# Performance work log

Hardware: AMD Instinct MI355X
Metric: run time of the kernel (lower is better)

Reference implementation:

```python
import jax, jax.numpy as jnp
import numpy as np

N_NODES = 50000
N_EDGES = 800000
N_GRAPHS = 1024
N_PAIRS = 16384
N_CL = 16
IN_CH = 64
EMB = 128
HID = 256
OUT = 1


def _xavier(key, shape):
    fan_in, fan_out = shape[-2], shape[-1]
    lim = (6.0 / (fan_in + fan_out)) ** 0.5
    return jax.random.uniform(key, shape, jnp.float32, -lim, lim)


def setup_inputs() -> dict:
    key = jax.random.key(0)
    ks = jax.random.split(key, 12)
    x = jax.random.normal(ks[0], (N_NODES, IN_CH), jnp.float32)
    edge_index = jax.random.randint(ks[1], (2, N_EDGES), 0, N_NODES)
    batch = jnp.sort(jax.random.randint(ks[2], (N_NODES,), 0, N_GRAPHS))
    drug_drug_batch = jax.random.randint(ks[3], (2, N_PAIRS), 0, N_GRAPHS)
    edge_cell_lines = jax.random.randint(ks[4], (N_PAIRS,), 0, N_CL)
    conv1_w = _xavier(ks[5], (IN_CH, EMB))
    conv2_w = _xavier(ks[6], (EMB, EMB))
    reg_w1 = _xavier(ks[7], (N_CL, 2 * EMB, HID))
    reg_w2 = _xavier(ks[8], (N_CL, HID, OUT))
    return dict(
        x=x,
        conv1_w=conv1_w, conv1_b=jnp.zeros((EMB,), jnp.float32),
        conv2_w=conv2_w, conv2_b=jnp.zeros((EMB,), jnp.float32),
        reg_w1=reg_w1, reg_b1=jnp.zeros((N_CL, HID), jnp.float32),
        reg_w2=reg_w2, reg_b2=jnp.zeros((N_CL, OUT), jnp.float32),
        edge_index=edge_index, batch=batch,
        drug_drug_batch=drug_drug_batch, edge_cell_lines=edge_cell_lines,
    )


def _forward(x, conv1_w, conv1_b, conv2_w, conv2_b,
             reg_w1, reg_b1, reg_w2, reg_b2,
             edge_index, batch, drug_drug_batch, edge_cell_lines):
    n = x.shape[0]
    # GCN normalization with self-loops (PyG GCNConv default)
    loop = jnp.arange(n)
    row = jnp.concatenate([edge_index[0], loop])  # source
    col = jnp.concatenate([edge_index[1], loop])  # target
    deg = jax.ops.segment_sum(jnp.ones(row.shape[0], x.dtype), col, num_segments=n)
    dinv = jnp.where(deg > 0, jax.lax.rsqrt(deg), 0.0)
    norm = dinv[row] * dinv[col]  # [E+N]

    def gcn(h, W, b):
        hw = h @ W
        agg = jax.ops.segment_sum(norm[:, None] * hw[row], col, num_segments=n)
        return agg + b

    h = jax.nn.relu(gcn(x, conv1_w, conv1_b))
    h = jax.nn.relu(gcn(h, conv2_w, conv2_b))

    # scatter-mean pooling over graphs
    gsum = jax.ops.segment_sum(h, batch, num_segments=N_GRAPHS)
    cnt = jax.ops.segment_sum(jnp.ones(n, h.dtype), batch, num_segments=N_GRAPHS)
    graph_embeds = gsum / jnp.maximum(cnt, 1.0)[:, None]

    # np.digitize(ddb, unique(ddb)+1); with contiguous ids 0..G-1 this is identity,
    # expressed faithfully via searchsorted against bins = arange(G)+1
    bins = jnp.arange(N_GRAPHS) + 1
    q = jnp.searchsorted(bins, drug_drug_batch, side='right')
    pair = jnp.concatenate([graph_embeds[q[0]], graph_embeds[q[1]]], axis=1)  # [P, 2*EMB]

    # per-cell-line Linear-ReLU-Linear, computed for all lines then selected
    hcl = jax.nn.relu(jnp.einsum('pe,ceh->pch', pair, reg_w1) + reg_b1[None])  # [P,C,H]
    ocl = jnp.einsum('pch,cho->pco', hcl, reg_w2) + reg_b2[None]               # [P,C,O]
    preds = jnp.take_along_axis(ocl, edge_cell_lines[:, None, None], axis=1)[:, 0, :]
    return preds


def reference(x, conv1_w, conv1_b, conv2_w, conv2_b,
              reg_w1, reg_b1, reg_w2, reg_b2,
              edge_index, batch, drug_drug_batch, edge_cell_lines):
    return _forward(x, conv1_w, conv1_b, conv2_w, conv2_b,
                    reg_w1, reg_b1, reg_w2, reg_b2,
                    edge_index, batch, drug_drug_batch, edge_cell_lines)
```

## Files before the change

### kernel.cpp

```cpp
#include <hip/hip_runtime.h>
#include <hip/hip_fp16.h>

#define NN 50000
#define NE 800000
#define NG 1024
#define NP 16384
#define NCL 16
#define INCH 64
#define EMB 128
#define HID 256

#define NB 391
#define NCHUNK 400
#define EPB 2000

#define CDIV(a,b) (((a)+(b)-1)/(b))

typedef _Float16 f16x8 __attribute__((ext_vector_type(8)));
typedef float    f32x4 __attribute__((ext_vector_type(4)));

template<int NW>
__device__ __forceinline__ int block_excl_scan(int v, int t, int* incl_out) {
    int lane = t & 63, w = t >> 6;
    int s = v;
#pragma unroll
    for (int d = 1; d < 64; d <<= 1) {
        int u = __shfl_up(s, d, 64);
        if (lane >= d) s += u;
    }
    __shared__ int wsum[NW];
    if (lane == 63) wsum[w] = s;
    __syncthreads();
    int add = 0;
    for (int k = 0; k < w; ++k) add += wsum[k];
    *incl_out = s + add;
    return s + add - v;
}

__global__ __launch_bounds__(256) void k_cnt(const int* __restrict__ cols,
                                             int* __restrict__ cnt) {
    __shared__ int hist[NB];
    int ch = blockIdx.x, t = threadIdx.x;
    for (int b = t; b < NB; b += 256) hist[b] = 0;
    __syncthreads();
    for (int e = ch * EPB + t; e < (ch + 1) * EPB; e += 256)
        atomicAdd(&hist[cols[e] >> 7], 1);
    __syncthreads();
    for (int b = t; b < NB; b += 256) cnt[b * NCHUNK + ch] = hist[b];
}

__global__ __launch_bounds__(512) void k_bscan(int* __restrict__ cnt,
                                               int* __restrict__ btot) {
    int b = blockIdx.x, t = threadIdx.x;
    int v = (t < NCHUNK) ? cnt[b * NCHUNK + t] : 0;
    int incl;
    int excl = block_excl_scan<8>(v, t, &incl);
    if (t < NCHUNK) cnt[b * NCHUNK + t] = excl;
    if (t == NCHUNK - 1) btot[b] = incl;
}

__global__ __launch_bounds__(512) void k_btot(const int* __restrict__ btot,
                                              int* __restrict__ bbase) {
    int t = threadIdx.x;
    int v = (t < NB) ? btot[t] : 0;
    int incl;
    int excl = block_excl_scan<8>(v, t, &incl);
    if (t < NB) bbase[t] = excl;
    if (t == NB - 1) bbase[NB] = incl;
}

__global__ __launch_bounds__(256) void k_part(const int* __restrict__ rows,
                                              const int* __restrict__ cols,
                                              const int* __restrict__ cnt,
                                              const int* __restrict__ bbase,
                                              int* __restrict__ ebuf) {
    __shared__ int cur[NB];
    int ch = blockIdx.x, t = threadIdx.x;
    for (int b = t; b < NB; b += 256) cur[b] = bbase[b] + cnt[b * NCHUNK + ch];
    __syncthreads();
    for (int e = ch * EPB + t; e < (ch + 1) * EPB; e += 256) {
        int c = cols[e], r = rows[e];
        int pos = atomicAdd(&cur[c >> 7], 1);
        ebuf[pos] = (r << 7) | (c & 127);
    }
}

__global__ __launch_bounds__(256) void k_bsort(const int* __restrict__ ebuf,
                                               const int* __restrict__ bbase,
                                               const float* __restrict__ x,
                                               int* __restrict__ off,
                                               float* __restrict__ dinv,
                                               int* __restrict__ srows,
                                               __half* __restrict__ xs) {
    __shared__ int   ldeg[128];
    __shared__ int   lcur[128];
    __shared__ float ldinv[128];
    int b = blockIdx.x, t = threadIdx.x;
    int n0 = b << 7;
    int nloc = min(128, NN - n0);
    int beg = bbase[b], end = bbase[b + 1];
    if (t < 128) ldeg[t] = 0;
    __syncthreads();
    for (int i = beg + t; i < end; i += 256)
        atomicAdd(&ldeg[ebuf[i] & 127], 1);
    __syncthreads();
    int v = (t < nloc) ? ldeg[t] : 0;
    int incl;
    int excl = block_excl_scan<4>(v, t, &incl);
    if (t < nloc) {
        off[n0 + t]  = beg + excl + v;
        float d = rsqrtf((float)(v + 1));
        dinv[n0 + t] = d;
        ldinv[t] = d;
        lcur[t] = beg + excl;
    }
    __syncthreads();
    for (int i = beg + t; i < end; i += 256) {
        int e = ebuf[i];
        int pos = atomicAdd(&lcur[e & 127], 1);
        srows[pos] = e >> 7;
    }
    const float4* Xx = (const float4*)x;
#pragma unroll
    for (int i = 0; i < 8; ++i) {
        int f4 = t + i * 256;
        int rloc = f4 >> 4, kq = f4 & 15;
        if (rloc < nloc) {
            float d = ldinv[rloc];
            float4 vv = Xx[(size_t)(n0 + rloc) * 16 + kq];
            __half2 h[2];
            h[0] = __floats2half2_rn(d * vv.x, d * vv.y);
            h[1] = __floats2half2_rn(d * vv.z, d * vv.w);
            ((float2*)xs)[(size_t)(n0 + rloc) * 16 + kq] = *(float2*)h;
        }
    }
}

__global__ __launch_bounds__(256) void k_wconv(const float* __restrict__ W,
                                               __half* __restrict__ WT, int K) {
    int i = blockIdx.x * 256 + threadIdx.x;
    if (i >= K * 128) return;
    int k = i >> 7, n = i & 127;
    WT[n * K + k] = __float2half(W[i]);
}

__global__ __launch_bounds__(256) void k_wconvb(const float* __restrict__ W1,
                                                __half* __restrict__ Whl) {
    int i = blockIdx.x * 256 + threadIdx.x;
    if (i >= 32 * 256 * 16) return;
    int ch = i & 15, tg = (i >> 4) & 255, z = i >> 12;
    int c = z >> 1, part = z & 1;
    f16x8 hi, lo;
#pragma unroll
    for (int j = 0; j < 8; ++j) {
        float v = W1[(size_t)c * 65536 + (size_t)(part * 128 + ch * 8 + j) * 256 + tg];
        _Float16 h = (_Float16)v;
        hi[j] = h;
        lo[j] = (_Float16)(v - (float)h);
    }
    size_t base = ((size_t)z * 256 + tg) * 16 + ch;
    ((f16x8*)Whl)[base] = hi;
    ((f16x8*)Whl)[(size_t)32 * 256 * 16 + base] = lo;
}

template<int FEAT, bool ZB>
__global__ __launch_bounds__(256) void k_gath_h(const int* __restrict__ off,
                                                const int* __restrict__ srows,
                                                const float* __restrict__ dinv,
                                                const __half* __restrict__ SRC,
                                                __half* __restrict__ DST,
                                                float* __restrict__ zbuf) {
    if (ZB) {
        if (blockIdx.x < 512) zbuf[(blockIdx.x << 8) + threadIdx.x] = 0.f;
    }
    constexpr int NC = FEAT / 8;
    constexpr int PL = NC / 8;
    int node = blockIdx.x * 4 + (threadIdx.x >> 6);
    int lane = threadIdx.x & 63;
    int slot = lane >> 3, q = lane & 7;
    if (node >= NN) return;
    int beg = node ? off[node - 1] : 0;
    int end = off[node];
    float di = dinv[node];
    const float4* S4 = (const float4*)SRC;

    float acc[PL][8];
#pragma unroll
    for (int i = 0; i < PL; ++i)
#pragma unroll
        for (int j = 0; j < 8; ++j) acc[i][j] = 0.f;

    if (slot == 0) {
#pragma unroll
        for (int i = 0; i < PL; ++i) {
            float4 raw = S4[node * NC + i * 8 + q];
            const __half2* h = (const __half2*)&raw;
#pragma unroll
            for (int j = 0; j < 4; ++j) {
                float2 f = __half22float2(h[j]);
                acc[i][2 * j + 0] = f.x;
                acc[i][2 * j + 1] = f.y;
            }
        }
    }
    for (int e = beg + slot; e < end; e += 8) {
        int r = srows[e];
#pragma unroll
        for (int i = 0; i < PL; ++i) {
            float4 raw = S4[r * NC + i * 8 + q];
            const __half2* h = (const __half2*)&raw;
#pragma unroll
            for (int j = 0; j < 4; ++j) {
                float2 f = __half22float2(h[j]);
                acc[i][2 * j + 0] += f.x;
                acc[i][2 * j + 1] += f.y;
            }
        }
    }
#pragma unroll
    for (int d = 8; d < 64; d <<= 1)
#pragma unroll
        for (int i = 0; i < PL; ++i)
#pragma unroll
            for (int j = 0; j < 8; ++j)
                acc[i][j] += __shfl_xor(acc[i][j], d, 64);

    if (lane < 8) {
        float4* D4 = (float4*)DST;
#pragma unroll
        for (int i = 0; i < PL; ++i) {
            float4 pk;
            __half2* hp = (__half2*)&pk;
            hp[0] = __floats2half2_rn(di * acc[i][0], di * acc[i][1]);
            hp[1] = __floats2half2_rn(di * acc[i][2], di * acc[i][3]);
            hp[2] = __floats2half2_rn(di * acc[i][4], di * acc[i][5]);
            hp[3] = __floats2half2_rn(di * acc[i][6], di * acc[i][7]);
            D4[node * NC + i * 8 + lane] = pk;
        }
    }
}

template<int K, bool RS, bool POOL>
__global__ __launch_bounds__(256) void gemm_mf(const __half* __restrict__ X,
                                               const __half* __restrict__ WT,
                                               const float* __restrict__ bias,
                                               const float* __restrict__ rs,
                                               const int* __restrict__ batch,
                                               float* __restrict__ Y, int M) {
    constexpr int KP = K + 8;
    __shared__ __half Xs[64 * KP];
    __shared__ __half Ws[128 * KP];
    __shared__ int sb[64];
    const int t = threadIdx.x;
    const int row0 = blockIdx.x * 64;

    const float4* X8 = (const float4*)X;
#pragma unroll
    for (int i = t; i < 64 * (K / 8); i += 256) {
        int r = i / (K / 8), ch = i % (K / 8);
        float4 v = make_float4(0.f, 0.f, 0.f, 0.f);
        if (row0 + r < M) v = X8[(size_t)(row0 + r) * (K / 8) + ch];
        *(float4*)&Xs[r * KP + ch * 8] = v;
    }
    const float4* W8 = (const float4*)WT;
#pragma unroll
    for (int i = t; i < 128 * (K / 8); i += 256) {
        int n = i / (K / 8), ch = i % (K / 8);
        *(float4*)&Ws[n * KP + ch * 8] = W8[i];
    }
    if (POOL) {
        if (t < 64) sb[t] = (row0 + t < M) ? batch[row0 + t] : -1;
    }
    __syncthreads();

    const int w  = t >> 6;
    const int l  = t & 63;
    const int lm = l & 15, lg = l >> 4;

    f32x4 acc[8];
#pragma unroll
    for (int c = 0; c < 8; ++c) acc[c] = (f32x4){0.f, 0.f, 0.f, 0.f};

#pragma unroll
    for (int kk = 0; kk < K / 32; ++kk) {
        f16x8 a = *(const f16x8*)&Xs[(16 * w + lm) * KP + kk * 32 + lg * 8];
#pragma unroll
        for (int c = 0; c < 8; ++c) {
            f16x8 bf = *(const f16x8*)&Ws[(16 * c + lm) * KP + kk * 32 + lg * 8];
            acc[c] = __builtin_amdgcn_mfma_f32_16x16x32_f16(a, bf, acc[c], 0, 0, 0);
        }
    }

    float bcol[8];
#pragma unroll
    for (int c = 0; c < 8; ++c) bcol[c] = bias[16 * c + lm];

    if (POOL) {
#pragma unroll
        for (int c = 0; c < 8; ++c) {
            int rung = -1;
            float run = 0.f;
#pragma unroll
            for (int j = 0; j < 4; ++j) {
                int rr = 16 * w + 4 * lg + j;
                int g = (row0 + rr < M) ? sb[rr] : -1;
                if (g != rung) {
                    if (rung >= 0) atomicAdd(&Y[rung * 128 + 16 * c + lm], run);
                    run = 0.f;
                    rung = g;
                }
                if (g >= 0) run += fmaxf(acc[c][j] + bcol[c], 0.f);
            }
            if (rung >= 0) atomicAdd(&Y[rung * 128 + 16 * c + lm], run);
        }
        return;
    }

    __half* Yh = (__half*)Y;
#pragma unroll
    for (int j = 0; j < 4; ++j) {
        int r = row0 + 16 * w + 4 * lg + j;
        if (r < M) {
            float d = RS ? rs[r] : 1.f;
#pragma unroll
            for (int c = 0; c < 8; ++c) {
                float v = d * fmaxf(acc[c][j] + bcol[c], 0.f);
                Yh[(size_t)r * 128 + 16 * c + lm] = __float2half(v);
            }
        }
    }
}

__global__ __launch_bounds__(128) void k_div(const float* __restrict__ gsum,
                                             const int* __restrict__ batch,
                                             __half* __restrict__ geh) {
    int g = blockIdx.x;
    __shared__ float inv;
    if (threadIdx.x == 0) {
        int lo = 0, hi = NN;
        while (lo < hi) { int m = (lo + hi) >> 1; if (batch[m] < g) lo = m + 1; else hi = m; }
        int s = lo;
        lo = 0; hi = NN;
        while (lo < hi) { int m = (lo + hi) >> 1; if (batch[m] < g + 1) lo = m + 1; else hi = m; }
        float c = (float)(lo - s);
        inv = 1.f / fmaxf(c, 1.f);
    }
    __syncthreads();
    geh[g * 128 + threadIdx.x] = __float2half(gsum[g * 128 + threadIdx.x] * inv);
}

__global__ __launch_bounds__(256) void gemm_bat(const __half* __restrict__ GEh,
                                                const __half* __restrict__ Whl,
                                                float* __restrict__ Aarr,
                                                float* __restrict__ Barr) {
    constexpr int KP = 128 + 8;
    __shared__ __half Xs[64 * KP];
    __shared__ __half Ws[128 * KP];
    const int t = threadIdx.x;
    const int row0 = blockIdx.x * 64;
    const int y = blockIdx.y, z = blockIdx.z;

    const float4* X8 = (const float4*)GEh;
#pragma unroll
    for (int i = t; i < 64 * 16; i += 256) {
        int r = i >> 4, ch = i & 15;
        *(float4*)&Xs[r * KP + ch * 8] = X8[(size_t)(row0 + r) * 16 + ch];
    }

    const int w  = t >> 6;
    const int l  = t & 63;
    const int lm = l & 15, lg = l >> 4;

    f32x4 acc[8];
#pragma unroll
    for (int c = 0; c < 8; ++c) acc[c] = (f32x4){0.f, 0.f, 0.f, 0.f};

    const float4* W8 = (const float4*)Whl;
#pragma unroll
    for (int pass = 0; pass < 2; ++pass) {
        __syncthreads();
        size_t wbase = ((size_t)pass * 32 + z) * 256 * 16;
#pragma unroll
        for (int i = t; i < 128 * 16; i += 256) {
            int n = i >> 4, ch = i & 15;
            *(float4*)&Ws[n * KP + ch * 8] = W8[wbase + (size_t)(y * 128 + n) * 16 + ch];
        }
        __syncthreads();
#pragma unroll
        for (int kk = 0; kk < 4; ++kk) {
            f16x8 a = *(const f16x8*)&Xs[(16 * w + lm) * KP + kk * 32 + lg * 8];
#pragma unroll
            for (int c = 0; c < 8; ++c) {
                f16x8 bf = *(const f16x8*)&Ws[(16 * c + lm) * KP + kk * 32 + lg * 8];
                acc[c] = __builtin_amdgcn_mfma_f32_16x16x32_f16(a, bf, acc[c], 0, 0, 0);
            }
        }
    }

    float* Obase = (z & 1) ? Barr : Aarr;
#pragma unroll
    for (int j = 0; j < 4; ++j) {
        int g = row0 + 16 * w + 4 * lg + j;
        size_t rb = ((size_t)(z >> 1) * NG + g) * HID + y * 128;
#pragma unroll
        for (int c = 0; c < 8; ++c)
            Obase[rb + 16 * c + lm] = acc[c][j];
    }
}

__global__ __launch_bounds__(256) void k_pair(const float* __restrict__ Aarr,
                                              const float* __restrict__ Barr,
                                              const int* __restrict__ ddb,
                                              const int* __restrict__ ecl,
                                              const float* __restrict__ B1,
                                              const float* __restrict__ W2,
                                              const float* __restrict__ B2,
                                              float* __restrict__ out) {
    int p = blockIdx.x * 4 + (threadIdx.x >> 6);
    int lane = threadIdx.x & 63;
    int c = ecl[p];
    int a = ddb[p];
    int b = ddb[NP + p];
    const float4* rA = (const float4*)&Aarr[((size_t)c * NG + a) * HID];
    const float4* rB = (const float4*)&Barr[((size_t)c * NG + b) * HID];
    const float4* b1 = (const float4*)&B1[c * HID];
    const float4* w2 = (const float4*)&W2[c * HID];
    float4 va = rA[lane], vb = rB[lane], v1 = b1[lane], v2 = w2[lane];
    float hx = va.x + vb.x + v1.x;
    float hy = va.y + vb.y + v1.y;
    float hz = va.z + vb.z + v1.z;
    float hw = va.w + vb.w + v1.w;
    float s = 0.f;
    s = fmaf(hx > 0.f ? hx : 0.f, v2.x, s);
    s = fmaf(hy > 0.f ? hy : 0.f, v2.y, s);
    s = fmaf(hz > 0.f ? hz : 0.f, v2.z, s);
    s = fmaf(hw > 0.f ? hw : 0.f, v2.w, s);
    for (int o = 32; o; o >>= 1) s += __shfl_down(s, o, 64);
    if (lane == 0) out[p] = s + B2[c];
}

extern "C" void kernel_launch(void* const* d_in, const int* in_sizes, int n_in,
                              void* d_out, int out_size, void* d_ws, size_t ws_size,
                              hipStream_t stream) {
    const float* x    = (const float*)d_in[0];
    const float* c1w  = (const float*)d_in[1];
    const float* c1b  = (const float*)d_in[2];
    const float* c2w  = (const float*)d_in[3];
    const float* c2b  = (const float*)d_in[4];
    const float* rw1  = (const float*)d_in[5];
    const float* rb1  = (const float*)d_in[6];
    const float* rw2  = (const float*)d_in[7];
    const float* rb2  = (const float*)d_in[8];
    const int*   eidx = (const int*)d_in[9];
    const int*   batch= (const int*)d_in[10];
    const int*   ddb  = (const int*)d_in[11];
    const int*   ecl  = (const int*)d_in[12];
    float* out = (float*)d_out;

    int*   off   = (int*)d_ws;
    int*   srows = off + 50048;
    float* dinv  = (float*)(srows + NE);
    float* bufA  = dinv + 50048;
    float* bufB  = bufA + NN * EMB;

    int*    ebuf  = (int*)bufA;
    int*    cnt   = (int*)(bufB + 1700000);
    int*    btot  = cnt + NB * NCHUNK;
    int*    bbase = btot + 512;
    __half* xs    = (__half*)bufB;
    __half* aggXh = (__half*)bufA;
    __half* H1h   = (__half*)bufB;
    __half* aggHh = (__half*)bufA;
    float*  gsum  = bufA + 4500000;
    __half* w1t   = (__half*)(bufA + 4700000);
    __half* w2t   = (__half*)(bufA + 4710000);
    __half* geh   = (__half*)(bufA + 4720000);
    __half* Whl   = (__half*)(bufB + 4300000);
    float*  Aarr  = bufA;
    float*  Barr  = bufB;

    const int* erow = eidx;
    const int* ecol = eidx + NE;

    k_wconv<<<CDIV(INCH*128,256),256,0,stream>>>(c1w, w1t, INCH);
    k_wconv<<<CDIV(EMB*128,256),256,0,stream>>>(c2w, w2t, EMB);
    k_wconvb<<<CDIV(32*256*16,256),256,0,stream>>>(rw1, Whl);

    k_cnt  <<<NCHUNK, 256, 0, stream>>>(ecol, cnt);
    k_bscan<<<NB,     512, 0, stream>>>(cnt, btot);
    k_btot <<<1,      512, 0, stream>>>(btot, bbase);
    k_part <<<NCHUNK, 256, 0, stream>>>(erow, ecol, cnt, bbase, ebuf);
    k_bsort<<<NB,     256, 0, stream>>>(ebuf, bbase, x, off, dinv, srows, xs);

    k_gath_h<INCH,true><<<CDIV(NN,4),256,0,stream>>>(off, srows, dinv, xs, aggXh, gsum);
    gemm_mf<INCH,true,false><<<CDIV(NN,64),256,0,stream>>>(aggXh, w1t, c1b, dinv, nullptr, (float*)H1h, NN);

    k_gath_h<EMB,false><<<CDIV(NN,4),256,0,stream>>>(off, srows, dinv, H1h, aggHh, nullptr);
    gemm_mf<EMB,false,true><<<CDIV(NN,64),256,0,stream>>>(aggHh, w2t, c2b, nullptr, batch, gsum, NN);
    k_div<<<NG,128,0,stream>>>(gsum, batch, geh);

    dim3 bgrid(NG/64, 2, 2*NCL);
    gemm_bat<<<bgrid,256,0,stream>>>(geh, Whl, Aarr, Barr);
    k_pair<<<NP/4,256,0,stream>>>(Aarr, Barr, ddb, ecl, rb1, rw2, rb2, out);
}
```

Measured before the change: 171.9 us.

## Merge prep kernels, fold scans and mean division, sort 16-bit neighbor lists

Merges the three weight-conversion kernels and the per-graph count computation into one prep launch. The block-total scan moves into k_part, and the mean division moves into the gemm_bat load, which removes the k_btot and k_div launches. Neighbor row indices are stored as 16-bit values (node ids are below 65536), and each node's list is insertion-sorted in shared memory so the later gathers read rows in more local order. The trade-off is redundant scan work in every k_part block, a serial per-thread insertion sort, and a large shared-memory buffer in k_bsort.

```diff
diff --git a/kernel.cpp b/kernel.cpp
--- a/kernel.cpp
+++ b/kernel.cpp
@@ -13,11 +13,13 @@
 #define NB 391
 #define NCHUNK 400
 #define EPB 2000
+#define SEDGE_CAP 6144
 
 #define CDIV(a,b) (((a)+(b)-1)/(b))
 
 typedef _Float16 f16x8 __attribute__((ext_vector_type(8)));
 typedef float    f32x4 __attribute__((ext_vector_type(4)));
+typedef unsigned short ushort_t;
 
 template<int NW>
 __device__ __forceinline__ int block_excl_scan(int v, int t, int* incl_out) {
@@ -35,6 +37,50 @@
     for (int k = 0; k < w; ++k) add += wsum[k];
     *incl_out = s + add;
     return s + add - v;
+}
+
+__global__ __launch_bounds__(256) void k_prep(const float* __restrict__ c1w,
+                                              const float* __restrict__ c2w,
+                                              const float* __restrict__ rw1,
+                                              const int* __restrict__ batch,
+                                              __half* __restrict__ w1t,
+                                              __half* __restrict__ w2t,
+                                              __half* __restrict__ Whl,
+                                              float* __restrict__ inv) {
+    int bid = blockIdx.x, t = threadIdx.x;
+    if (bid < 512) {
+        int i = bid * 256 + t;
+        int ch = i & 15, tg = (i >> 4) & 255, z = i >> 12;
+        int c = z >> 1, part = z & 1;
+        f16x8 hi, lo;
+#pragma unroll
+        for (int j = 0; j < 8; ++j) {
+            float v = rw1[(size_t)c * 65536 + (size_t)(part * 128 + ch * 8 + j) * 256 + tg];
+            _Float16 h = (_Float16)v;
+            hi[j] = h;
+            lo[j] = (_Float16)(v - (float)h);
+        }
+        size_t base = ((size_t)z * 256 + tg) * 16 + ch;
+        ((f16x8*)Whl)[base] = hi;
+        ((f16x8*)Whl)[(size_t)32 * 256 * 16 + base] = lo;
+    } else if (bid < 544) {
+        int i = (bid - 512) * 256 + t;
+        int k = i >> 7, n = i & 127;
+        w1t[n * INCH + k] = __float2half(c1w[i]);
+    } else if (bid < 608) {
+        int i = (bid - 544) * 256 + t;
+        int k = i >> 7, n = i & 127;
+        w2t[n * EMB + k] = __float2half(c2w[i]);
+    } else {
+        int g = (bid - 608) * 256 + t;
+        int lo_ = 0, hi_ = NN;
+        while (lo_ < hi_) { int m = (lo_ + hi_) >> 1; if (batch[m] < g) lo_ = m + 1; else hi_ = m; }
+        int s = lo_;
+        lo_ = 0; hi_ = NN;
+        while (lo_ < hi_) { int m = (lo_ + hi_) >> 1; if (batch[m] < g + 1) lo_ = m + 1; else hi_ = m; }
+        float c = (float)(lo_ - s);
+        inv[g] = 1.f / fmaxf(c, 1.f);
+    }
 }
 
 __global__ __launch_bounds__(256) void k_cnt(const int* __restrict__ cols,
@@ -59,24 +105,30 @@
     if (t == NCHUNK - 1) btot[b] = incl;
 }
 
-__global__ __launch_bounds__(512) void k_btot(const int* __restrict__ btot,
-                                              int* __restrict__ bbase) {
-    int t = threadIdx.x;
-    int v = (t < NB) ? btot[t] : 0;
-    int incl;
-    int excl = block_excl_scan<8>(v, t, &incl);
-    if (t < NB) bbase[t] = excl;
-    if (t == NB - 1) bbase[NB] = incl;
-}
-
 __global__ __launch_bounds__(256) void k_part(const int* __restrict__ rows,
                                               const int* __restrict__ cols,
                                               const int* __restrict__ cnt,
-                                              const int* __restrict__ bbase,
+                                              const int* __restrict__ btot,
+                                              int* __restrict__ bbase_out,
                                               int* __restrict__ ebuf) {
+    __shared__ int bb[NB + 1];
     __shared__ int cur[NB];
+    __shared__ int S0s;
     int ch = blockIdx.x, t = threadIdx.x;
-    for (int b = t; b < NB; b += 256) cur[b] = bbase[b] + cnt[b * NCHUNK + ch];
+    int incl;
+    int v0 = btot[t];
+    int e0 = block_excl_scan<4>(v0, t, &incl);
+    bb[t] = e0;
+    if (t == 255) S0s = incl;
+    __syncthreads();
+    int t2 = t + 256;
+    int v1 = (t2 < NB) ? btot[t2] : 0;
+    int e1 = block_excl_scan<4>(v1, t, &incl);
+    if (t2 <= NB) bb[t2] = e1 + S0s;
+    __syncthreads();
+    for (int b = t; b < NB; b += 256) cur[b] = bb[b] + cnt[b * NCHUNK + ch];
+    if (ch == 0)
+        for (int i = t; i <= NB; i += 256) bbase_out[i] = bb[i];
     __syncthreads();
     for (int e = ch * EPB + t; e < (ch + 1) * EPB; e += 256) {
         int c = cols[e], r = rows[e];
@@ -90,15 +142,18 @@
                                                const float* __restrict__ x,
                                                int* __restrict__ off,
                                                float* __restrict__ dinv,
-                                               int* __restrict__ srows,
+                                               ushort_t* __restrict__ srows,
                                                __half* __restrict__ xs) {
-    __shared__ int   ldeg[128];
-    __shared__ int   lcur[128];
-    __shared__ float ldinv[128];
+    __shared__ int      ldeg[128];
+    __shared__ int      lcur[128];
+    __shared__ float    ldinv[128];
+    __shared__ ushort_t sedge[SEDGE_CAP];
     int b = blockIdx.x, t = threadIdx.x;
     int n0 = b << 7;
     int nloc = min(128, NN - n0);
     int beg = bbase[b], end = bbase[b + 1];
+    int ne = end - beg;
+    bool fits = (ne <= SEDGE_CAP);
     if (t < 128) ldeg[t] = 0;
     __syncthreads();
     for (int i = beg + t; i < end; i += 256)
@@ -107,18 +162,36 @@
     int v = (t < nloc) ? ldeg[t] : 0;
     int incl;
     int excl = block_excl_scan<4>(v, t, &incl);
+    int myoff = excl, mydeg = v;
     if (t < nloc) {
         off[n0 + t]  = beg + excl + v;
         float d = rsqrtf((float)(v + 1));
         dinv[n0 + t] = d;
         ldinv[t] = d;
-        lcur[t] = beg + excl;
+        lcur[t] = excl;
     }
     __syncthreads();
     for (int i = beg + t; i < end; i += 256) {
         int e = ebuf[i];
         int pos = atomicAdd(&lcur[e & 127], 1);
-        srows[pos] = e >> 7;
+        if (fits) sedge[pos] = (ushort_t)(e >> 7);
+        else      srows[beg + pos] = (ushort_t)(e >> 7);
+    }
+    __syncthreads();
+    if (fits) {
+        if (t < nloc) {
+            for (int i = 1; i < mydeg; ++i) {
+                ushort_t key = sedge[myoff + i];
+                int j = i - 1;
+                while (j >= 0 && sedge[myoff + j] > key) {
+                    sedge[myoff + j + 1] = sedge[myoff + j];
+                    --j;
+                }
+                sedge[myoff + j + 1] = key;
+            }
+        }
+        __syncthreads();
+        for (int i = t; i < ne; i += 256) srows[beg + i] = sedge[i];
     }
     const float4* Xx = (const float4*)x;
 #pragma unroll
@@ -136,36 +209,9 @@
     }
 }
 
-__global__ __launch_bounds__(256) void k_wconv(const float* __restrict__ W,
-                                               __half* __restrict__ WT, int K) {
-    int i = blockIdx.x * 256 + threadIdx.x;
-    if (i >= K * 128) return;
-    int k = i >> 7, n = i & 127;
-    WT[n * K + k] = __float2half(W[i]);
-}
-
-__global__ __launch_bounds__(256) void k_wconvb(const float* __restrict__ W1,
-                                                __half* __restrict__ Whl) {
-    int i = blockIdx.x * 256 + threadIdx.x;
-    if (i >= 32 * 256 * 16) return;
-    int ch = i & 15, tg = (i >> 4) & 255, z = i >> 12;
-    int c = z >> 1, part = z & 1;
-    f16x8 hi, lo;
-#pragma unroll
-    for (int j = 0; j < 8; ++j) {
-        float v = W1[(size_t)c * 65536 + (size_t)(part * 128 + ch * 8 + j) * 256 + tg];
-        _Float16 h = (_Float16)v;
-        hi[j] = h;
-        lo[j] = (_Float16)(v - (float)h);
-    }
-    size_t base = ((size_t)z * 256 + tg) * 16 + ch;
-    ((f16x8*)Whl)[base] = hi;
-    ((f16x8*)Whl)[(size_t)32 * 256 * 16 + base] = lo;
-}
-
 template<int FEAT, bool ZB>
 __global__ __launch_bounds__(256) void k_gath_h(const int* __restrict__ off,
-                                                const int* __restrict__ srows,
+                                                const ushort_t* __restrict__ srows,
                                                 const float* __restrict__ dinv,
                                                 const __half* __restrict__ SRC,
                                                 __half* __restrict__ DST,
@@ -331,25 +377,8 @@
     }
 }
 
-__global__ __launch_bounds__(128) void k_div(const float* __restrict__ gsum,
-                                             const int* __restrict__ batch,
-                                             __half* __restrict__ geh) {
-    int g = blockIdx.x;
-    __shared__ float inv;
-    if (threadIdx.x == 0) {
-        int lo = 0, hi = NN;
-        while (lo < hi) { int m = (lo + hi) >> 1; if (batch[m] < g) lo = m + 1; else hi = m; }
-        int s = lo;
-        lo = 0; hi = NN;
-        while (lo < hi) { int m = (lo + hi) >> 1; if (batch[m] < g + 1) lo = m + 1; else hi = m; }
-        float c = (float)(lo - s);
-        inv = 1.f / fmaxf(c, 1.f);
-    }
-    __syncthreads();
-    geh[g * 128 + threadIdx.x] = __float2half(gsum[g * 128 + threadIdx.x] * inv);
-}
-
-__global__ __launch_bounds__(256) void gemm_bat(const __half* __restrict__ GEh,
+__global__ __launch_bounds__(256) void gemm_bat(const float* __restrict__ gsum,
+                                                const float* __restrict__ inv,
                                                 const __half* __restrict__ Whl,
                                                 float* __restrict__ Aarr,
                                                 float* __restrict__ Barr) {
@@ -360,11 +389,21 @@
     const int row0 = blockIdx.x * 64;
     const int y = blockIdx.y, z = blockIdx.z;
 
-    const float4* X8 = (const float4*)GEh;
+    const float4* G4 = (const float4*)gsum;
 #pragma unroll
     for (int i = t; i < 64 * 16; i += 256) {
         int r = i >> 4, ch = i & 15;
-        *(float4*)&Xs[r * KP + ch * 8] = X8[(size_t)(row0 + r) * 16 + ch];
+        int g = row0 + r;
+        float iv = inv[g];
+        float4 a = G4[g * 32 + ch * 2];
+        float4 b4 = G4[g * 32 + ch * 2 + 1];
+        float4 pk;
+        __half2* hp = (__half2*)&pk;
+        hp[0] = __floats2half2_rn(iv * a.x, iv * a.y);
+        hp[1] = __floats2half2_rn(iv * a.z, iv * a.w);
+        hp[2] = __floats2half2_rn(iv * b4.x, iv * b4.y);
+        hp[3] = __floats2half2_rn(iv * b4.z, iv * b4.w);
+        *(float4*)&Xs[r * KP + ch * 8] = pk;
     }
 
     const int w  = t >> 6;
@@ -463,43 +502,40 @@
     float* bufA  = dinv + 50048;
     float* bufB  = bufA + NN * EMB;
 
-    int*    ebuf  = (int*)bufA;
-    int*    cnt   = (int*)(bufB + 1700000);
-    int*    btot  = cnt + NB * NCHUNK;
-    int*    bbase = btot + 512;
-    __half* xs    = (__half*)bufB;
-    __half* aggXh = (__half*)bufA;
-    __half* H1h   = (__half*)bufB;
-    __half* aggHh = (__half*)bufA;
-    float*  gsum  = bufA + 4500000;
-    __half* w1t   = (__half*)(bufA + 4700000);
-    __half* w2t   = (__half*)(bufA + 4710000);
-    __half* geh   = (__half*)(bufA + 4720000);
-    __half* Whl   = (__half*)(bufB + 4300000);
-    float*  Aarr  = bufA;
-    float*  Barr  = bufB;
+    int*      ebuf  = (int*)bufA;
+    int*      cnt   = (int*)(bufB + 1700000);
+    int*      btot  = cnt + NB * NCHUNK;
+    int*      bbase = btot + 512;
+    __half*   xs    = (__half*)bufB;
+    __half*   aggXh = (__half*)bufA;
+    __half*   H1h   = (__half*)bufB;
+    __half*   aggHh = (__half*)bufA;
+    float*    gsum  = bufA + 4500000;
+    __half*   w1t   = (__half*)(bufA + 4700000);
+    __half*   w2t   = (__half*)(bufA + 4710000);
+    float*    inv   = bufA + 4730000;
+    __half*   Whl   = (__half*)(bufB + 4300000);
+    float*    Aarr  = bufA;
+    float*    Barr  = bufB;
+    ushort_t* srowsU = (ushort_t*)srows;
 
     const int* erow = eidx;
     const int* ecol = eidx + NE;
 
-    k_wconv<<<CDIV(INCH*128,256),256,0,stream>>>(c1w, w1t, INCH);
-    k_wconv<<<CDIV(EMB*128,256),256,0,stream>>>(c2w, w2t, EMB);
-    k_wconvb<<<CDIV(32*256*16,256),256,0,stream>>>(rw1, Whl);
+    k_prep<<<612, 256, 0, stream>>>(c1w, c2w, rw1, batch, w1t, w2t, Whl, inv);
 
     k_cnt  <<<NCHUNK, 256, 0, stream>>>(ecol, cnt);
     k_bscan<<<NB,     512, 0, stream>>>(cnt, btot);
-    k_btot <<<1,      512, 0, stream>>>(btot, bbase);
-    k_part <<<NCHUNK, 256, 0, stream>>>(erow, ecol, cnt, bbase, ebuf);
-    k_bsort<<<NB,     256, 0, stream>>>(ebuf, bbase, x, off, dinv, srows, xs);
-
-    k_gath_h<INCH,true><<<CDIV(NN,4),256,0,stream>>>(off, srows, dinv, xs, aggXh, gsum);
+    k_part <<<NCHUNK, 256, 0, stream>>>(erow, ecol, cnt, btot, bbase, ebuf);
+    k_bsort<<<NB,     256, 0, stream>>>(ebuf, bbase, x, off, dinv, srowsU, xs);
+
+    k_gath_h<INCH,true><<<CDIV(NN,4),256,0,stream>>>(off, srowsU, dinv, xs, aggXh, gsum);
     gemm_mf<INCH,true,false><<<CDIV(NN,64),256,0,stream>>>(aggXh, w1t, c1b, dinv, nullptr, (float*)H1h, NN);
 
-    k_gath_h<EMB,false><<<CDIV(NN,4),256,0,stream>>>(off, srows, dinv, H1h, aggHh, nullptr);
+    k_gath_h<EMB,false><<<CDIV(NN,4),256,0,stream>>>(off, srowsU, dinv, H1h, aggHh, nullptr);
     gemm_mf<EMB,false,true><<<CDIV(NN,64),256,0,stream>>>(aggHh, w2t, c2b, nullptr, batch, gsum, NN);
-    k_div<<<NG,128,0,stream>>>(gsum, batch, geh);
 
     dim3 bgrid(NG/64, 2, 2*NCL);
-    gemm_bat<<<bgrid,256,0,stream>>>(geh, Whl, Aarr, Barr);
+    gemm_bat<<<bgrid,256,0,stream>>>(gsum, inv, Whl, Aarr, Barr);
     k_pair<<<NP/4,256,0,stream>>>(Aarr, Barr, ddb, ecl, rb1, rw2, rb2, out);
 }
```

Measured after the change: 202.1 us. 1.18x slower.
